# Kernel tuning notes

Measured on AMD Instinct MI355X. Metric: run time of the kernel, lower is better.

## Reference

```python
import jax, jax.numpy as jnp
import numpy as np

VOXEL_SIZE = np.array([0.1, 0.1, 0.2], np.float32)
PC_RANGE = np.array([-51.2, -51.2, -5.0, 51.2, 51.2, 3.0], np.float32)
MAX_POINTS = 32
MAX_VOXELS = 60000  # training cap (max_voxels[0])
GRID = np.round((PC_RANGE[3:] - PC_RANGE[:3]) / VOXEL_SIZE).astype(np.int64)  # [1024,1024,40]
N_POINTS = 1_200_000


def setup_inputs() -> dict:
    key = jax.random.key(0)
    k1, k2 = jax.random.split(key)
    lo = jnp.asarray(PC_RANGE[:3] - 2.0)   # slight margin -> some out-of-range points get dropped
    hi = jnp.asarray(PC_RANGE[3:] + 2.0)
    xyz = jax.random.uniform(k1, (N_POINTS, 3), minval=lo, maxval=hi)
    feat = jax.random.uniform(k2, (N_POINTS, 1))  # reflectivity
    return {"points": jnp.concatenate([xyz, feat], axis=1)}


def reference(points):
    # Hard voxelization (deterministic): first-occurrence voxel ordering,
    # first max_points points kept per voxel, capped at max_voxels.
    # Outputs padded to static MAX_VOXELS; voxel_num gives the valid count.
    N, ndim = points.shape
    gx, gy, gz = int(GRID[0]), int(GRID[1]), int(GRID[2])
    sentinel = gx * gy * gz  # flat id for out-of-range points (sorts last)

    vs = jnp.asarray(VOXEL_SIZE)
    rmin = jnp.asarray(PC_RANGE[:3])
    c = jnp.floor((points[:, :3] - rmin) / vs).astype(jnp.int32)  # [N,3] (x,y,z)
    valid = jnp.all((c >= 0) & (c < jnp.asarray(GRID, jnp.int32)), axis=1)
    flat = jnp.where(valid, (c[:, 0] * gy + c[:, 1]) * gz + c[:, 2], sentinel)

    # stable sort -> within a voxel, points keep original order
    order = jnp.argsort(flat, stable=True)
    sflat = flat[order]
    svalid = valid[order]

    new_seg = jnp.concatenate([jnp.array([True]), sflat[1:] != sflat[:-1]])
    seg_id = jnp.cumsum(new_seg) - 1                      # segment index per sorted point
    pos = jnp.arange(N)
    seg_start = jax.lax.cummax(jnp.where(new_seg, pos, 0), axis=0)
    rank = pos - seg_start                                # slot of point within its voxel

    seg_rep = jax.ops.segment_min(order, seg_id, num_segments=N)          # first-occurrence point idx
    seg_count = jax.ops.segment_sum(svalid.astype(jnp.int32), seg_id, num_segments=N)
    seg_exists = seg_count > 0                            # real (in-range) voxel segments

    # order voxels by first occurrence (matches deterministic CUDA kernel)
    rep_key = jnp.where(seg_exists, seg_rep, N)
    vox_order = jnp.argsort(rep_key, stable=True)
    vid = jnp.zeros(N, jnp.int32).at[vox_order].set(jnp.arange(N, dtype=jnp.int32))

    # scatter points into [MAX_VOXELS, MAX_POINTS, ndim]
    pv = vid[seg_id]
    keep = svalid & (pv < MAX_VOXELS) & (rank < MAX_POINTS)
    pv_s = jnp.where(keep, pv, MAX_VOXELS)  # OOB -> dropped
    voxels = jnp.zeros((MAX_VOXELS, MAX_POINTS, ndim), points.dtype)
    voxels = voxels.at[pv_s, jnp.minimum(rank, MAX_POINTS - 1)].set(points[order], mode='drop')

    # per-voxel outputs
    seg_vid = jnp.where(seg_exists, vid, MAX_VOXELS)
    npv = jnp.zeros(MAX_VOXELS, jnp.int32).at[seg_vid].set(
        jnp.minimum(seg_count, MAX_POINTS), mode='drop')
    seg_flat = jax.ops.segment_min(sflat, seg_id, num_segments=N)
    zc = seg_flat % gz
    yc = (seg_flat // gz) % gy
    xc = seg_flat // (gy * gz)
    coors = jnp.zeros((MAX_VOXELS, 3), jnp.int32).at[seg_vid].set(
        jnp.stack([zc, yc, xc], axis=1).astype(jnp.int32), mode='drop')  # (z, y, x) like mmcv

    voxel_num = jnp.minimum(jnp.sum(seg_exists.astype(jnp.int32)), MAX_VOXELS)
    return voxels, coors, npv, voxel_num
```

## Files before the change

### kernel.cpp

```cpp
#include <hip/hip_runtime.h>
#include <stdint.h>


#define GX 1024
#define GY 1024
#define GZ 40
#define NVOXEL (GX * GY * GZ)
#define MAXV 60000
#define MAXP 32
#define HBITS 21
#define HSIZE (1u << HBITS)
#define HMASK (HSIZE - 1u)
#define CANDBIT (1 << 30)
#define FLATMASK (CANDBIT - 1)
#define TB 256
#define KEARLY 131072
#define NBE (KEARLY / TB)
#define NBITW (NVOXEL / 32)
#define EMPTY64 0xFFFFFFFFFFFFFFFFull

#define OFF_COORS ((size_t)MAXV * MAXP * 4)
#define OFF_NPV   (OFF_COORS + (size_t)MAXV * 3)
#define OFF_VNUM  (OFF_NPV + (size_t)MAXV)

typedef unsigned long long u64;

__device__ __forceinline__ unsigned hashf(int flat) {
    return ((unsigned)flat * 2654435761u) >> (32 - HBITS);
}

__global__ void k_init(u64* __restrict__ h64, unsigned char* __restrict__ contested,
                       int* __restrict__ dupcnt, int* __restrict__ repidx,
                       int n, float* __restrict__ oF, int* __restrict__ nvox,
                       unsigned* __restrict__ bitmap, unsigned* __restrict__ dcnt) {
    int i = blockIdx.x * blockDim.x + threadIdx.x;
    int stride = gridDim.x * blockDim.x;
    if (i == 0) { *nvox = 0; *dcnt = 0; }
    for (int j = i; j < (int)HSIZE; j += stride) h64[j] = EMPTY64;
    for (int j = i; j < NBITW; j += stride) bitmap[j] = 0u;
    int nw = (n + 3) / 4;
    unsigned* c4 = (unsigned*)contested;
    for (int j = i; j < nw; j += stride) c4[j] = 0;
    for (int j = i; j < MAXV; j += stride) { dupcnt[j] = 0; repidx[j] = -1; }
    for (int j = i; j < MAXV * 3; j += stride) oF[OFF_COORS + j] = 0.f;
}

__device__ __forceinline__ int voxel_flat(float4 pt) {
    float fx = floorf((pt.x + 51.2f) / 0.1f);
    float fy = floorf((pt.y + 51.2f) / 0.1f);
    float fz = floorf((pt.z + 5.0f) / 0.2f);
    int cx = (int)fx, cy = (int)fy, cz = (int)fz;
    bool valid = (fx >= 0.f) & (cx < GX) & (fy >= 0.f) & (cy < GY) & (fz >= 0.f) & (cz < GZ);
    return valid ? (cx * GY + cy) * GZ + cz : -1;
}

__device__ __forceinline__ int build_insert(int p, int flat, u64* __restrict__ h64,
                                            unsigned char* __restrict__ contested,
                                            int* __restrict__ nvox,
                                            unsigned* __restrict__ bitmap,
                                            int count_wins) {
    u64 want = ((u64)(unsigned)flat << 32) | (unsigned)p;
    unsigned slot = hashf(flat);
    int cand = 0, won = 0;
    for (int probe = 0; probe < 4096; probe++) {
        u64 cur = atomicCAS(&h64[slot], EMPTY64, want);
        if (cur == EMPTY64) { cand = 1; won = 1; break; }
        if ((unsigned)(cur >> 32) == (unsigned)flat) {
            if ((unsigned)cur > (unsigned)p) {
                u64 old = atomicMin(&h64[slot], want);
                unsigned oldrep = (unsigned)old;
                if (oldrep > (unsigned)p) {
                    contested[oldrep] = 1;
                    cand = 1;
                }
            }
            break;
        }
        slot = (slot + 1u) & HMASK;
    }
    if (won) {
        atomicOr(&bitmap[(unsigned)flat >> 5], 1u << (flat & 31));
        if (count_wins) atomicAdd(nvox, 1);
    }
    return flat | (cand ? CANDBIT : 0);
}

__global__ __launch_bounds__(TB) void k_build_early(const float4* __restrict__ pts, int nE,
                                                    u64* __restrict__ h64,
                                                    int* __restrict__ pflat,
                                                    unsigned char* __restrict__ contested,
                                                    int* __restrict__ nvox,
                                                    unsigned* __restrict__ bitmap) {
    int p = blockIdx.x * blockDim.x + threadIdx.x;
    if (p >= nE) return;
    float4 pt = pts[p];
    int flat = voxel_flat(pt);
    if (flat < 0) { pflat[p] = -1; return; }
    pflat[p] = build_insert(p, flat, h64, contested, nvox, bitmap, 1);
}

__global__ __launch_bounds__(TB) void k_build_late(const float4* __restrict__ pts, int n,
                                                   u64* __restrict__ h64,
                                                   int* __restrict__ pflat,
                                                   unsigned char* __restrict__ contested,
                                                   int* __restrict__ nvox,
                                                   unsigned* __restrict__ bitmap,
                                                   u64* __restrict__ latedup,
                                                   unsigned* __restrict__ dcnt) {
    int p = KEARLY + blockIdx.x * blockDim.x + threadIdx.x;
    if (p >= n) return;
    float4 pt = pts[p];
    int flat = voxel_flat(pt);
    if (*nvox < MAXV) {
        if (flat < 0) { pflat[p] = -1; return; }
        pflat[p] = build_insert(p, flat, h64, contested, nvox, bitmap, 0);
        return;
    }
    if (flat < 0) return;
    unsigned w = bitmap[(unsigned)flat >> 5];
    if (w & (1u << (flat & 31))) {
        unsigned pos = atomicAdd(dcnt, 1u);
        if (pos < (unsigned)(n - KEARLY))
            latedup[pos] = ((u64)(unsigned)flat << 32) | (unsigned)p;
    }
}

__global__ __launch_bounds__(TB) void k_flags(const int* __restrict__ pflat,
                                              const unsigned char* __restrict__ contested,
                                              int n, u64* __restrict__ flagbits,
                                              int* __restrict__ partials,
                                              const int* __restrict__ nvox) {
    __shared__ int ws[4];
    int b = blockIdx.x, t = threadIdx.x;
    int i = b * TB + t;
    int fastmode = (*nvox >= MAXV);
    int pred = 0;
    if (i < n && (b < NBE || !fastmode)) {
        int pf = pflat[i];
        pred = (pf >= 0) && (pf & CANDBIT) && !contested[i];
    }
    u64 m = __ballot(pred);
    int w = t >> 6, lane = t & 63;
    if (lane == 0) { flagbits[b * 4 + w] = m; ws[w] = __popcll(m); }
    __syncthreads();
    if (t == 0) partials[b] = ws[0] + ws[1] + ws[2] + ws[3];
}

__global__ __launch_bounds__(1024) void k_scan(int* __restrict__ partials, int npart,
                                               float* __restrict__ oF) {
    __shared__ int sh[1024];
    int t = threadIdx.x;
    int v[5];
    int s = 0;
    #pragma unroll
    for (int k = 0; k < 5; k++) {
        int idx = t * 5 + k;
        v[k] = (idx < npart) ? partials[idx] : 0;
        s += v[k];
    }
    sh[t] = s;
    __syncthreads();
    for (int off = 1; off < 1024; off <<= 1) {
        int add = (t >= off) ? sh[t - off] : 0;
        __syncthreads();
        sh[t] += add;
        __syncthreads();
    }
    int run = sh[t] - s;
    #pragma unroll
    for (int k = 0; k < 5; k++) {
        int idx = t * 5 + k;
        if (idx < npart) partials[idx] = run;
        run += v[k];
    }
    if (t == 1023) {
        int total = sh[1023];
        if (total > MAXV) total = MAXV;
        oF[OFF_VNUM] = (float)total;
    }
}

__device__ __forceinline__ void register_dup(int flat, int i,
                                             const u64* __restrict__ h64,
                                             const u64* __restrict__ flagbits,
                                             const int* __restrict__ partials,
                                             int* __restrict__ dupcnt,
                                             int* __restrict__ list) {
    unsigned slot = hashf(flat);
    unsigned rep = 0xFFFFFFFFu;
    for (int probe = 0; probe < 4096; probe++) {
        u64 cur = h64[slot];
        if ((unsigned)(cur >> 32) == (unsigned)flat) { rep = (unsigned)cur; break; }
        if (cur == EMPTY64) break;
        slot = (slot + 1u) & HMASK;
    }
    if (rep == 0xFFFFFFFFu) return;
    int br = (int)(rep >> 8);
    int lb = (int)(rep & 255u);
    int dvid = partials[br];
    int wb = br * 4, nw = lb >> 6;
    for (int q = 0; q < nw; q++) dvid += (int)__popcll(flagbits[wb + q]);
    int tail = lb & 63;
    if (tail) dvid += (int)__popcll(flagbits[wb + nw] & ((1ull << tail) - 1ull));
    if (dvid < MAXV) {
        int pos = atomicAdd(&dupcnt[dvid], 1);
        if (pos < MAXP - 1) list[dvid * (MAXP - 1) + pos] = i;
    }
}

__global__ __launch_bounds__(TB) void k_finish(const u64* __restrict__ flagbits,
                                               const int* __restrict__ partials,
                                               const int* __restrict__ pflat,
                                               const u64* __restrict__ h64,
                                               int* __restrict__ repidx,
                                               int* __restrict__ dupcnt,
                                               int* __restrict__ list, int n,
                                               float* __restrict__ oF,
                                               const int* __restrict__ nvox,
                                               const u64* __restrict__ latedup,
                                               const unsigned* __restrict__ dcnt) {
    int b = blockIdx.x, t = threadIdx.x;
    int fastmode = (*nvox >= MAXV);
    if (fastmode && b >= NBE) {
        unsigned cnt = *dcnt;
        unsigned cap = (unsigned)(n - KEARLY);
        if (cnt > cap) cnt = cap;
        unsigned idx = (unsigned)(b - NBE) * TB + t;
        if (idx < cnt) {
            u64 e = latedup[idx];
            register_dup((int)(e >> 32), (int)(unsigned)e,
                         h64, flagbits, partials, dupcnt, list);
        }
        return;
    }
    int i = b * TB + t;
    if (i >= n) return;
    int lane = t & 63, w = t >> 6;
    u64 w0 = flagbits[b * 4 + 0];
    u64 w1 = flagbits[b * 4 + 1];
    u64 w2 = flagbits[b * 4 + 2];
    u64 w3 = flagbits[b * 4 + 3];
    u64 myw = (w == 0) ? w0 : (w == 1) ? w1 : (w == 2) ? w2 : w3;
    int bit = (int)((myw >> lane) & 1);
    int pf = pflat[i];
    if (bit) {
        int wbase = (w > 0 ? __popcll(w0) : 0) + (w > 1 ? __popcll(w1) : 0)
                  + (w > 2 ? __popcll(w2) : 0);
        int vid = partials[b] + wbase + (int)__popcll(myw & ((1ull << lane) - 1ull));
        if (vid < MAXV) {
            int flat = pf & FLATMASK;
            int zc = flat % GZ;
            int t2 = flat / GZ;
            int yc = t2 % GY;
            int xc = t2 / GY;
            size_t cOff = OFF_COORS + (size_t)vid * 3;
            oF[cOff + 0] = (float)zc;
            oF[cOff + 1] = (float)yc;
            oF[cOff + 2] = (float)xc;
            repidx[vid] = i;
        }
    } else if (pf >= 0) {
        register_dup(pf & FLATMASK, i, h64, flagbits, partials, dupcnt, list);
    }
}

__global__ __launch_bounds__(TB) void k_emit(const float4* __restrict__ pts,
                                             const int* __restrict__ repidx,
                                             const int* __restrict__ dupcnt,
                                             const int* __restrict__ list,
                                             float4* __restrict__ outVox,
                                             float* __restrict__ oF) {
    int gid = blockIdx.x * TB + threadIdx.x;
    int vid = gid >> 5;
    if (vid >= MAXV) return;
    int r = gid & 31;
    int ri = repidx[vid];
    int dc = dupcnt[vid];
    int d = dc < (MAXP - 1) ? dc : (MAXP - 1);
    int m = (ri >= 0) ? (1 + d) : 0;
    if (r == 0) oF[OFF_NPV + vid] = (float)m;
    float4 row = make_float4(0.f, 0.f, 0.f, 0.f);
    if (r == 0 && m > 0) {
        row = pts[ri];
    } else if (r < m) {
        const int* lst = &list[vid * (MAXP - 1)];
        int target = r - 1, pick = -1;
        for (int a = 0; a < d; a++) {
            int e = lst[a];
            int rk = 0;
            for (int bq = 0; bq < d; bq++) rk += (lst[bq] < e);
            if (rk == target) pick = e;
        }
        row = pts[pick];
    }
    outVox[(size_t)vid * MAXP + r] = row;
}

extern "C" void kernel_launch(void* const* d_in, const int* in_sizes, int n_in,
                              void* d_out, int out_size, void* d_ws, size_t ws_size,
                              hipStream_t stream) {
    int n = in_sizes[0] / 4;
    const float4* pts = (const float4*)d_in[0];

    int tb = TB;
    int nbp = (n + tb - 1) / tb;
    int nwords = nbp * 4;

    char* base = (char*)d_ws;
    size_t o = 0;
    int* partials = (int*)(base + o);  o += ((size_t)nbp * 4 + 255) & ~(size_t)255;
    int* dupcnt   = (int*)(base + o);  o += (size_t)MAXV * 4;
    int* repidx   = (int*)(base + o);  o += (size_t)MAXV * 4;
    o = (o + 255) & ~(size_t)255;
    u64* flagbits = (u64*)(base + o);  o += (size_t)nwords * 8;
    o = (o + 255) & ~(size_t)255;
    unsigned char* contested = (unsigned char*)(base + o);  o += ((size_t)n + 255) & ~(size_t)255;
    u64* h64      = (u64*)(base + o);  o += (size_t)HSIZE * 8;
    int* pflat    = (int*)(base + o);  o += (size_t)n * 4;
    int* list     = (int*)(base + o);  o += (size_t)MAXV * (MAXP - 1) * 4;
    o = (o + 255) & ~(size_t)255;
    unsigned* bitmap = (unsigned*)(base + o);  o += (size_t)NBITW * 4;
    o = (o + 255) & ~(size_t)255;
    u64* latedup  = (u64*)(base + o);  o += (size_t)(n > KEARLY ? n - KEARLY : 1) * 8;
    o = (o + 255) & ~(size_t)255;
    int* nvox     = (int*)(base + o);  o += 256;
    unsigned* dcnt = (unsigned*)(base + o);  o += 256;

    float* oF = (float*)d_out;

    int nE = n < KEARLY ? n : KEARLY;
    int nbE = (nE + tb - 1) / tb;
    int nL = n - nE;

    k_init<<<2048, tb, 0, stream>>>(h64, contested, dupcnt, repidx, n, oF, nvox,
                                    bitmap, dcnt);
    k_build_early<<<nbE, tb, 0, stream>>>(pts, nE, h64, pflat, contested, nvox, bitmap);
    if (nL > 0)
        k_build_late<<<(nL + tb - 1) / tb, tb, 0, stream>>>(pts, n, h64, pflat,
                                                            contested, nvox, bitmap,
                                                            latedup, dcnt);
    k_flags<<<nbp, tb, 0, stream>>>(pflat, contested, n, flagbits, partials, nvox);
    k_scan<<<1, 1024, 0, stream>>>(partials, nbp, oF);
    k_finish<<<nbp, tb, 0, stream>>>(flagbits, partials, pflat, h64, repidx, dupcnt,
                                     list, n, oF, nvox, latedup, dcnt);
    k_emit<<<(MAXV * MAXP + tb - 1) / tb, tb, 0, stream>>>(pts, repidx, dupcnt, list,
                                                           (float4*)d_out, oF);
}
```

Baseline: 140.0 us.

## Fuse late build, flag ballot and scan into one persistent kernel

Replaces the separate late-build, flag, and single-block scan kernels with one persistent 1024-block kernel. It uses a software grid barrier and last-block-done atomics so the scan runs inline. It also shrinks the hash table from 2^21 to 2^18 slots, which cuts init clearing traffic but raises load factor and probe lengths. The aim is fewer launches and less initialization, at the risk of spin-barrier overhead and deadlock if the blocks are not all co-resident.

After: 149.5 us. +6.8%, slower.

```diff
diff --git a/kernel.cpp b/kernel.cpp
--- a/kernel.cpp
+++ b/kernel.cpp
@@ -8,7 +8,7 @@
 #define NVOXEL (GX * GY * GZ)
 #define MAXV 60000
 #define MAXP 32
-#define HBITS 21
+#define HBITS 18
 #define HSIZE (1u << HBITS)
 #define HMASK (HSIZE - 1u)
 #define CANDBIT (1 << 30)
@@ -17,6 +17,8 @@
 #define KEARLY 131072
 #define NBE (KEARLY / TB)
 #define NBITW (NVOXEL / 32)
+#define MIDB 1024
+#define NREL 32
 #define EMPTY64 0xFFFFFFFFFFFFFFFFull
 
 #define OFF_COORS ((size_t)MAXV * MAXP * 4)
@@ -27,22 +29,6 @@
 
 __device__ __forceinline__ unsigned hashf(int flat) {
     return ((unsigned)flat * 2654435761u) >> (32 - HBITS);
-}
-
-__global__ void k_init(u64* __restrict__ h64, unsigned char* __restrict__ contested,
-                       int* __restrict__ dupcnt, int* __restrict__ repidx,
-                       int n, float* __restrict__ oF, int* __restrict__ nvox,
-                       unsigned* __restrict__ bitmap, unsigned* __restrict__ dcnt) {
-    int i = blockIdx.x * blockDim.x + threadIdx.x;
-    int stride = gridDim.x * blockDim.x;
-    if (i == 0) { *nvox = 0; *dcnt = 0; }
-    for (int j = i; j < (int)HSIZE; j += stride) h64[j] = EMPTY64;
-    for (int j = i; j < NBITW; j += stride) bitmap[j] = 0u;
-    int nw = (n + 3) / 4;
-    unsigned* c4 = (unsigned*)contested;
-    for (int j = i; j < nw; j += stride) c4[j] = 0;
-    for (int j = i; j < MAXV; j += stride) { dupcnt[j] = 0; repidx[j] = -1; }
-    for (int j = i; j < MAXV * 3; j += stride) oF[OFF_COORS + j] = 0.f;
 }
 
 __device__ __forceinline__ int voxel_flat(float4 pt) {
@@ -85,101 +71,6 @@
     return flat | (cand ? CANDBIT : 0);
 }
 
-__global__ __launch_bounds__(TB) void k_build_early(const float4* __restrict__ pts, int nE,
-                                                    u64* __restrict__ h64,
-                                                    int* __restrict__ pflat,
-                                                    unsigned char* __restrict__ contested,
-                                                    int* __restrict__ nvox,
-                                                    unsigned* __restrict__ bitmap) {
-    int p = blockIdx.x * blockDim.x + threadIdx.x;
-    if (p >= nE) return;
-    float4 pt = pts[p];
-    int flat = voxel_flat(pt);
-    if (flat < 0) { pflat[p] = -1; return; }
-    pflat[p] = build_insert(p, flat, h64, contested, nvox, bitmap, 1);
-}
-
-__global__ __launch_bounds__(TB) void k_build_late(const float4* __restrict__ pts, int n,
-                                                   u64* __restrict__ h64,
-                                                   int* __restrict__ pflat,
-                                                   unsigned char* __restrict__ contested,
-                                                   int* __restrict__ nvox,
-                                                   unsigned* __restrict__ bitmap,
-                                                   u64* __restrict__ latedup,
-                                                   unsigned* __restrict__ dcnt) {
-    int p = KEARLY + blockIdx.x * blockDim.x + threadIdx.x;
-    if (p >= n) return;
-    float4 pt = pts[p];
-    int flat = voxel_flat(pt);
-    if (*nvox < MAXV) {
-        if (flat < 0) { pflat[p] = -1; return; }
-        pflat[p] = build_insert(p, flat, h64, contested, nvox, bitmap, 0);
-        return;
-    }
-    if (flat < 0) return;
-    unsigned w = bitmap[(unsigned)flat >> 5];
-    if (w & (1u << (flat & 31))) {
-        unsigned pos = atomicAdd(dcnt, 1u);
-        if (pos < (unsigned)(n - KEARLY))
-            latedup[pos] = ((u64)(unsigned)flat << 32) | (unsigned)p;
-    }
-}
-
-__global__ __launch_bounds__(TB) void k_flags(const int* __restrict__ pflat,
-                                              const unsigned char* __restrict__ contested,
-                                              int n, u64* __restrict__ flagbits,
-                                              int* __restrict__ partials,
-                                              const int* __restrict__ nvox) {
-    __shared__ int ws[4];
-    int b = blockIdx.x, t = threadIdx.x;
-    int i = b * TB + t;
-    int fastmode = (*nvox >= MAXV);
-    int pred = 0;
-    if (i < n && (b < NBE || !fastmode)) {
-        int pf = pflat[i];
-        pred = (pf >= 0) && (pf & CANDBIT) && !contested[i];
-    }
-    u64 m = __ballot(pred);
-    int w = t >> 6, lane = t & 63;
-    if (lane == 0) { flagbits[b * 4 + w] = m; ws[w] = __popcll(m); }
-    __syncthreads();
-    if (t == 0) partials[b] = ws[0] + ws[1] + ws[2] + ws[3];
-}
-
-__global__ __launch_bounds__(1024) void k_scan(int* __restrict__ partials, int npart,
-                                               float* __restrict__ oF) {
-    __shared__ int sh[1024];
-    int t = threadIdx.x;
-    int v[5];
-    int s = 0;
-    #pragma unroll
-    for (int k = 0; k < 5; k++) {
-        int idx = t * 5 + k;
-        v[k] = (idx < npart) ? partials[idx] : 0;
-        s += v[k];
-    }
-    sh[t] = s;
-    __syncthreads();
-    for (int off = 1; off < 1024; off <<= 1) {
-        int add = (t >= off) ? sh[t - off] : 0;
-        __syncthreads();
-        sh[t] += add;
-        __syncthreads();
-    }
-    int run = sh[t] - s;
-    #pragma unroll
-    for (int k = 0; k < 5; k++) {
-        int idx = t * 5 + k;
-        if (idx < npart) partials[idx] = run;
-        run += v[k];
-    }
-    if (t == 1023) {
-        int total = sh[1023];
-        if (total > MAXV) total = MAXV;
-        oF[OFF_VNUM] = (float)total;
-    }
-}
-
 __device__ __forceinline__ void register_dup(int flat, int i,
                                              const u64* __restrict__ h64,
                                              const u64* __restrict__ flagbits,
@@ -205,6 +96,190 @@
     if (dvid < MAXV) {
         int pos = atomicAdd(&dupcnt[dvid], 1);
         if (pos < MAXP - 1) list[dvid * (MAXP - 1) + pos] = i;
+    }
+}
+
+__device__ __forceinline__ void scan_inline(int* __restrict__ partials, int npb,
+                                            float* __restrict__ oF) {
+    __shared__ int s2[TB];
+    int t = threadIdx.x;
+    int E = (npb + TB - 1) / TB;
+    int s = 0;
+    for (int k = 0; k < E; k++) {
+        int idx = t * E + k;
+        if (idx < npb) s += partials[idx];
+    }
+    s2[t] = s;
+    __syncthreads();
+    for (int off = 1; off < TB; off <<= 1) {
+        int add = (t >= off) ? s2[t - off] : 0;
+        __syncthreads();
+        s2[t] += add;
+        __syncthreads();
+    }
+    int run = s2[t] - s;
+    for (int k = 0; k < E; k++) {
+        int idx = t * E + k;
+        if (idx < npb) { int tmp = partials[idx]; partials[idx] = run; run += tmp; }
+    }
+    if (t == TB - 1) {
+        int total = s2[TB - 1];
+        if (total > MAXV) total = MAXV;
+        oF[OFF_VNUM] = (float)total;
+    }
+}
+
+__device__ __forceinline__ void fb_bar(int* __restrict__ ctrl) {
+    __shared__ int win;
+    __syncthreads();
+    if (threadIdx.x == 0) {
+        __threadfence();
+        int c = atomicAdd(&ctrl[16], 1);
+        win = (c == MIDB - 1);
+    }
+    __syncthreads();
+    if (win) {
+        if (threadIdx.x < NREL) atomicExch(&ctrl[32 + threadIdx.x * 16], 1);
+        __syncthreads();
+    } else {
+        if (threadIdx.x == 0) {
+            int* f = &ctrl[32 + (blockIdx.x & (NREL - 1)) * 16];
+            for (long sp = 0; sp < (1L << 24); sp++) {
+                if (atomicAdd(f, 0) != 0) break;
+                __builtin_amdgcn_s_sleep(2);
+            }
+        }
+        __syncthreads();
+    }
+    __threadfence();
+}
+
+__global__ void k_init(u64* __restrict__ h64, unsigned char* __restrict__ contested,
+                       int* __restrict__ dupcnt, int* __restrict__ repidx,
+                       int n, int nbp, float* __restrict__ oF,
+                       int* __restrict__ nvox, unsigned* __restrict__ bitmap,
+                       unsigned* __restrict__ dcnt, int* __restrict__ ctrl,
+                       int* __restrict__ partials) {
+    int i = blockIdx.x * blockDim.x + threadIdx.x;
+    int stride = gridDim.x * blockDim.x;
+    if (i == 0) { *nvox = 0; *dcnt = 0; }
+    for (int j = i; j < (int)HSIZE; j += stride) h64[j] = EMPTY64;
+    for (int j = i; j < NBITW; j += stride) bitmap[j] = 0u;
+    int nw = (n + 3) / 4;
+    unsigned* c4 = (unsigned*)contested;
+    for (int j = i; j < nw; j += stride) c4[j] = 0;
+    for (int j = i; j < MAXV; j += stride) { dupcnt[j] = 0; repidx[j] = -1; }
+    for (int j = i; j < MAXV * 3; j += stride) oF[OFF_COORS + j] = 0.f;
+    for (int j = i; j < nbp; j += stride) partials[j] = 0;
+    for (int j = i; j < 2048; j += stride) ctrl[j] = 0;
+}
+
+__global__ __launch_bounds__(TB) void k_build_early(const float4* __restrict__ pts, int nE,
+                                                    u64* __restrict__ h64,
+                                                    int* __restrict__ pflat,
+                                                    unsigned char* __restrict__ contested,
+                                                    int* __restrict__ nvox,
+                                                    unsigned* __restrict__ bitmap) {
+    int p = blockIdx.x * blockDim.x + threadIdx.x;
+    if (p >= nE) return;
+    float4 pt = pts[p];
+    int flat = voxel_flat(pt);
+    if (flat < 0) { pflat[p] = -1; return; }
+    pflat[p] = build_insert(p, flat, h64, contested, nvox, bitmap, 1);
+}
+
+__global__ __launch_bounds__(TB, 4) void k_mid(const float4* __restrict__ pts,
+                                               int n, int nbp,
+                                               u64* __restrict__ h64,
+                                               unsigned* __restrict__ bitmap,
+                                               unsigned char* __restrict__ contested,
+                                               int* __restrict__ pflat,
+                                               u64* __restrict__ flagbits,
+                                               int* __restrict__ partials,
+                                               u64* __restrict__ latedup,
+                                               int* __restrict__ nvox,
+                                               unsigned* __restrict__ dcnt,
+                                               int* __restrict__ ctrl,
+                                               float* __restrict__ oF) {
+    const int b = blockIdx.x, t = threadIdx.x;
+    const bool fast = (*nvox >= MAXV);
+    const int npbF = nbp < NBE ? nbp : NBE;
+    __shared__ int ws4[4];
+    __shared__ int amLast;
+
+    if (fast) {
+        if (b < npbF) {
+            int i = b * TB + t;
+            int pred = 0;
+            if (i < n) {
+                int pf = pflat[i];
+                pred = (pf >= 0) && (pf & CANDBIT) && !contested[i];
+            }
+            u64 m = __ballot(pred);
+            int w = t >> 6;
+            if ((t & 63) == 0) { flagbits[b * 4 + w] = m; ws4[w] = __popcll(m); }
+            __syncthreads();
+            if (t == 0) {
+                partials[b] = ws4[0] + ws4[1] + ws4[2] + ws4[3];
+                __threadfence();
+                int done = atomicAdd(&ctrl[0], 1);
+                amLast = (done == npbF - 1);
+            }
+            __syncthreads();
+            if (amLast) {
+                __threadfence();
+                scan_inline(partials, npbF, oF);
+            }
+        } else {
+            for (int p = KEARLY + (b - NBE) * TB + t; p < n; p += (MIDB - NBE) * TB) {
+                float4 pt = pts[p];
+                int flat = voxel_flat(pt);
+                if (flat < 0) continue;
+                unsigned wv = bitmap[(unsigned)flat >> 5];
+                if (wv & (1u << (flat & 31))) {
+                    unsigned pos = atomicAdd(dcnt, 1u);
+                    if (pos < (unsigned)(n - KEARLY))
+                        latedup[pos] = ((u64)(unsigned)flat << 32) | (unsigned)p;
+                }
+            }
+        }
+        return;
+    }
+
+    for (int p = KEARLY + b * TB + t; p < n; p += MIDB * TB) {
+        float4 pt = pts[p];
+        int flat = voxel_flat(pt);
+        if (flat < 0) { pflat[p] = -1; continue; }
+        pflat[p] = build_insert(p, flat, h64, contested, nvox, bitmap, 0);
+    }
+    fb_bar(ctrl);
+    for (int pb = b; pb < nbp; pb += MIDB) {
+        int i = pb * TB + t;
+        int pred = 0;
+        if (i < n) {
+            int pf = pflat[i];
+            pred = (pf >= 0) && (pf & CANDBIT) && !contested[i];
+        }
+        u64 m = __ballot(pred);
+        if ((t & 63) == 0) flagbits[pb * 4 + (t >> 6)] = m;
+        __syncthreads();
+        if (t == 0) {
+            int s = (int)__popcll(flagbits[pb * 4 + 0]) + (int)__popcll(flagbits[pb * 4 + 1])
+                  + (int)__popcll(flagbits[pb * 4 + 2]) + (int)__popcll(flagbits[pb * 4 + 3]);
+            partials[pb] = s;
+        }
+        __syncthreads();
+    }
+    __syncthreads();
+    if (t == 0) {
+        __threadfence();
+        int done = atomicAdd(&ctrl[8], 1);
+        amLast = (done == MIDB - 1);
+    }
+    __syncthreads();
+    if (amLast) {
+        __threadfence();
+        scan_inline(partials, nbp, oF);
     }
 }
 
@@ -223,7 +298,7 @@
     int fastmode = (*nvox >= MAXV);
     if (fastmode && b >= NBE) {
         unsigned cnt = *dcnt;
-        unsigned cap = (unsigned)(n - KEARLY);
+        unsigned cap = (n > KEARLY) ? (unsigned)(n - KEARLY) : 0u;
         if (cnt > cap) cnt = cap;
         unsigned idx = (unsigned)(b - NBE) * TB + t;
         if (idx < cnt) {
@@ -325,24 +400,21 @@
     o = (o + 255) & ~(size_t)255;
     int* nvox     = (int*)(base + o);  o += 256;
     unsigned* dcnt = (unsigned*)(base + o);  o += 256;
+    int* ctrl     = (int*)(base + o);  o += 2048 * 4;
 
     float* oF = (float*)d_out;
+    float4* outVox = (float4*)d_out;
 
     int nE = n < KEARLY ? n : KEARLY;
     int nbE = (nE + tb - 1) / tb;
-    int nL = n - nE;
-
-    k_init<<<2048, tb, 0, stream>>>(h64, contested, dupcnt, repidx, n, oF, nvox,
-                                    bitmap, dcnt);
+
+    k_init<<<2048, tb, 0, stream>>>(h64, contested, dupcnt, repidx, n, nbp, oF,
+                                    nvox, bitmap, dcnt, ctrl, partials);
     k_build_early<<<nbE, tb, 0, stream>>>(pts, nE, h64, pflat, contested, nvox, bitmap);
-    if (nL > 0)
-        k_build_late<<<(nL + tb - 1) / tb, tb, 0, stream>>>(pts, n, h64, pflat,
-                                                            contested, nvox, bitmap,
-                                                            latedup, dcnt);
-    k_flags<<<nbp, tb, 0, stream>>>(pflat, contested, n, flagbits, partials, nvox);
-    k_scan<<<1, 1024, 0, stream>>>(partials, nbp, oF);
+    k_mid<<<MIDB, tb, 0, stream>>>(pts, n, nbp, h64, bitmap, contested, pflat,
+                                   flagbits, partials, latedup, nvox, dcnt, ctrl, oF);
     k_finish<<<nbp, tb, 0, stream>>>(flagbits, partials, pflat, h64, repidx, dupcnt,
                                      list, n, oF, nvox, latedup, dcnt);
     k_emit<<<(MAXV * MAXP + tb - 1) / tb, tb, 0, stream>>>(pts, repidx, dupcnt, list,
-                                                           (float4*)d_out, oF);
-}
+                                                           outVox, oF);
+}
```
